# Kernel tuning notes

Hardware: AMD Instinct MI355X
Metric: run time of the kernel (lower is better)

The kernel has to match this reference:

```python
import jax, jax.numpy as jnp
import numpy as np

EPS = 1e-5


def setup_inputs() -> dict:
    key = jax.random.key(0)
    ks = jax.random.split(key, 8)
    B, C, D, H, O, E = 256, 64, 256, 4096, 256, 4
    x = jax.random.normal(ks[0], (B, C, D), dtype=jnp.float32)
    mask_ids = jax.random.randint(ks[1], (B, C), 0, 16)
    projection_idx = jax.random.randint(ks[2], (C,), 0, E)
    W1 = jax.random.normal(ks[3], (E, D, H), dtype=jnp.float32) * 0.02
    b1 = jnp.zeros((E, H), dtype=jnp.float32)
    gamma = jnp.ones((E, H), dtype=jnp.float32)
    beta = jnp.zeros((E, H), dtype=jnp.float32)
    W2 = jax.random.normal(ks[4], (E, H, O), dtype=jnp.float32) * 0.02
    b2 = jnp.zeros((E, O), dtype=jnp.float32)
    return {"x": x, "mask_ids": mask_ids, "projection_idx": projection_idx,
            "W1": W1, "b1": b1, "gamma": gamma, "beta": beta, "W2": W2, "b2": b2}


def reference(x, mask_ids, projection_idx, W1, b1, gamma, beta, W2, b2):
    # x: [B, C, D]; projection_idx: [C] routes each channel to one of E experts.
    # Disjoint masks => the original zeros + masked '+=' is a partition-assign.
    B, C, D = x.shape
    E, _, H = W1.shape
    # Per-channel expert params (gather once, shared over batch).
    h = jnp.einsum('bcd,cdh->bch', x, W1[projection_idx]) + b1[projection_idx]
    # BatchNorm1d in training mode: batch stats over the tokens of each expert
    # (the original flattens the selected [B, |mask|] tokens for BN).
    seg = jnp.broadcast_to(projection_idx[None, :], (B, C)).reshape(-1)  # [B*C]
    hf = h.reshape(B * C, H)
    cnt = jax.ops.segment_sum(jnp.ones((B * C,), h.dtype), seg, num_segments=E)
    cnt = jnp.maximum(cnt, 1.0)
    s1 = jax.ops.segment_sum(hf, seg, num_segments=E)            # [E, H]
    s2 = jax.ops.segment_sum(hf * hf, seg, num_segments=E)       # [E, H]
    mean = s1 / cnt[:, None]
    var = s2 / cnt[:, None] - mean * mean                        # biased var (train-mode BN)
    inv = jax.lax.rsqrt(var + EPS)
    hn = (h - mean[projection_idx]) * (inv[projection_idx] * gamma[projection_idx]) + beta[projection_idx]
    a = jax.nn.relu(hn)
    out = jnp.einsum('bch,cho->bco', a, W2[projection_idx]) + b2[projection_idx]
    return out, mask_ids
```

## Files before the change

kernel.cpp:

```cpp
#include <hip/hip_runtime.h>

typedef unsigned short u16;
typedef unsigned int   u32;
typedef __attribute__((ext_vector_type(8))) short s16x8;
typedef __attribute__((ext_vector_type(4))) float f32x4;
typedef __attribute__((ext_vector_type(4))) u32   u32x4;

#define DEV static __device__ __forceinline__

static constexpr int B_ = 256, C_ = 64, D_ = 256, H_ = 4096, O_ = 256, E_ = 4;

DEV u16 f2bf(float f) {
  u32 u = __builtin_bit_cast(u32, f);
  u += 0x7fffu + ((u >> 16) & 1u);
  return (u16)(u >> 16);
}
DEV float bf2f(u16 u) { return __builtin_bit_cast(float, (u32)u << 16); }

DEV void async16(const u16* g, u16* l) {
  __builtin_amdgcn_global_load_lds(
      (const __attribute__((address_space(1))) void*)g,
      (__attribute__((address_space(3))) void*)l, 16, 0, 0);
}

DEV int xcd_swz(int bid, int nwg) { return (bid & 7) * (nwg >> 3) + (bid >> 3); }

__global__ void k_prep(const float* __restrict__ x, u16* __restrict__ xb,
                       const float* __restrict__ W1, u16* __restrict__ w1t,
                       const float* __restrict__ W2, u16* __restrict__ w2t,
                       const int* __restrict__ mask, float* __restrict__ maskOut,
                       const int* __restrict__ proj, int* __restrict__ perm) {
  __shared__ float tile[64][65];
  const int bx = blockIdx.x, tid = threadIdx.x;
  if (bx < 2048) {
    const int i = bx * 256 + tid;
    const f32x4 a = ((const f32x4*)x)[2 * i];
    const f32x4 b = ((const f32x4*)x)[2 * i + 1];
    u32x4 o;
    o[0] = (u32)f2bf(a[0]) | ((u32)f2bf(a[1]) << 16);
    o[1] = (u32)f2bf(a[2]) | ((u32)f2bf(a[3]) << 16);
    o[2] = (u32)f2bf(b[0]) | ((u32)f2bf(b[1]) << 16);
    o[3] = (u32)f2bf(b[2]) | ((u32)f2bf(b[3]) << 16);
    ((u32x4*)xb)[i] = o;
    return;
  }
  if (bx < 4096) {
    const bool w1 = bx < 3072;
    const int R  = w1 ? D_ : H_;
    const int Cc = w1 ? H_ : O_;
    const float* s0 = w1 ? W1 : W2;
    u16* d0 = w1 ? w1t : w2t;
    int b = bx - (w1 ? 2048 : 3072);
    const int nct = Cc >> 6, nrt = R >> 6;
    const int ct = b % nct; b /= nct;
    const int rt = b % nrt; const int e = b / nrt;
    const float* s = s0 + (size_t)e * R * Cc;
    u16* d = d0 + (size_t)e * R * Cc;
    const int tx = tid & 63, ty = tid >> 6;
    #pragma unroll
    for (int i = 0; i < 64; i += 4)
      tile[i + ty][tx] = s[(size_t)(rt * 64 + i + ty) * Cc + ct * 64 + tx];
    __syncthreads();
    #pragma unroll
    for (int i = 0; i < 64; i += 4) {
      const int cc = i + ty;
      d[(size_t)(ct * 64 + cc) * R + rt * 64 + tx] = f2bf(tile[tx][cc]);
    }
    return;
  }
  if (bx < 4104) {
    const int i = (bx - 4096) * 256 + tid;
    #pragma unroll
    for (int j = 0; j < 8; ++j) maskOut[i * 8 + j] = (float)mask[i * 8 + j];
    return;
  }
  if (tid < C_) {
    const int e = proj[tid];
    int rank = 0;
    for (int c2 = 0; c2 < C_; ++c2) {
      const int e2 = proj[c2];
      rank += (e2 < e) || (e2 == e && c2 < tid);
    }
    perm[rank] = tid;
  }
}

__global__ __launch_bounds__(256, 3)
void k_gemm1(const u16* __restrict__ A, const u16* __restrict__ Bw,
             const int* __restrict__ proj, const int* __restrict__ perm,
             const float* __restrict__ bias,
             u16* __restrict__ outH, float* __restrict__ s1p, float* __restrict__ s2p) {
  constexpr int BM = 128, BN = 128, BK = 32, KT = D_ / BK;
  constexpr int SA = BM * BK / 8, SB = BN * BK / 8;
  constexpr int BUF = (SA + SB) * 8;
  __shared__ __align__(16) u16 lds[3 * BUF];
  __shared__ float stash[2][4][16][2];
  const int tid = threadIdx.x, l = tid & 63, w = tid >> 6, wm = w >> 1, wn = w & 1;

  int bid = xcd_swz(blockIdx.x, gridDim.x);
  constexpr int NT = H_ / BN, BT = B_ / BM;
  const int nt = bid % NT; bid /= NT;
  const int bt = bid % BT; const int ci = bid / BT;
  const int c = perm[ci];
  const int e = proj[c];

  const size_t rsA = (size_t)C_ * D_;
  const u16* Ab = A + (size_t)c * D_ + (size_t)bt * BM * rsA;
  const u16* Bb = Bw + ((size_t)e * H_ + (size_t)nt * BN) * D_;

  f32x4 acc[4][4] = {};

  auto stage = [&](int kt) {
    const int k0 = kt * BK;
    u16* dst = lds + (kt % 3) * BUF;
    #pragma unroll
    for (int i = 0; i < 2; ++i) {
      const int s = i * 256 + tid, row = s >> 2, j = (s & 3) ^ ((row >> 1) & 3);
      async16(Ab + (size_t)row * rsA + k0 + j * 8, dst + s * 8);
    }
    #pragma unroll
    for (int i = 0; i < 2; ++i) {
      const int s = i * 256 + tid, col = s >> 2, j = (s & 3) ^ ((col >> 1) & 3);
      async16(Bb + (size_t)col * D_ + k0 + j * 8, dst + SA * 8 + s * 8);
    }
  };

  stage(0);
  asm volatile("" ::: "memory");
  stage(1);
  asm volatile("s_waitcnt vmcnt(4)" ::: "memory");
  __builtin_amdgcn_s_barrier();

  #pragma unroll
  for (int kt = 0; kt < KT; ++kt) {
    if (kt + 2 < KT) stage(kt + 2);
    const u16* bufA = lds + (kt % 3) * BUF;
    const u16* bufB = bufA + SA * 8;
    s16x8 av[4], bv[4];
    #pragma unroll
    for (int m = 0; m < 4; ++m) {
      const int r = wm * 64 + m * 16 + (l & 15), p = (l >> 4) ^ ((r >> 1) & 3);
      av[m] = *(const s16x8*)(bufA + (r * 4 + p) * 8);
    }
    #pragma unroll
    for (int n = 0; n < 4; ++n) {
      const int cc = wn * 64 + n * 16 + (l & 15), p = (l >> 4) ^ ((cc >> 1) & 3);
      bv[n] = *(const s16x8*)(bufB + (cc * 4 + p) * 8);
    }
    #pragma unroll
    for (int m = 0; m < 4; ++m)
      #pragma unroll
      for (int n = 0; n < 4; ++n)
        acc[m][n] = __builtin_amdgcn_mfma_f32_16x16x32_bf16(av[m], bv[n], acc[m][n], 0, 0, 0);
    if (kt + 2 < KT)      asm volatile("s_waitcnt vmcnt(4) lgkmcnt(0)" ::: "memory");
    else if (kt + 1 < KT) asm volatile("s_waitcnt vmcnt(0) lgkmcnt(0)" ::: "memory");
    if (kt + 1 < KT) __builtin_amdgcn_s_barrier();
  }
  __syncthreads();

  u16* ldsOut = lds;
  float p1s[4], p2s[4];
  #pragma unroll
  for (int n = 0; n < 4; ++n) {
    const int colL = wn * 64 + n * 16 + (l & 15);
    const int colg = nt * BN + colL;
    const float bval = bias[e * H_ + colg];
    float p1 = 0.f, p2 = 0.f;
    #pragma unroll
    for (int m = 0; m < 4; ++m) {
      const int rbase = wm * 64 + m * 16 + (l >> 4) * 4;
      #pragma unroll
      for (int i = 0; i < 4; ++i) {
        const float v = acc[m][n][i] + bval;
        p1 += v; p2 += v * v;
        const int row = rbase + i;
        const int phys = (colL >> 3) ^ (row & 15);
        ldsOut[row * 128 + phys * 8 + (colL & 7)] = f2bf(v);
      }
    }
    p1 += __shfl_xor(p1, 16); p1 += __shfl_xor(p1, 32);
    p2 += __shfl_xor(p2, 16); p2 += __shfl_xor(p2, 32);
    if (wm == 1 && l < 16) { stash[wn][n][l & 15][0] = p1; stash[wn][n][l & 15][1] = p2; }
    p1s[n] = p1; p2s[n] = p2;
  }
  __syncthreads();
  if (wm == 0 && l < 16) {
    const int rowp = c * 2 + bt;
    #pragma unroll
    for (int n = 0; n < 4; ++n) {
      const int colg = nt * BN + wn * 64 + n * 16 + (l & 15);
      s1p[(size_t)rowp * H_ + colg] = p1s[n] + stash[wn][n][l & 15][0];
      s2p[(size_t)rowp * H_ + colg] = p2s[n] + stash[wn][n][l & 15][1];
    }
  }
  u16* outB = outH + (((size_t)c * NT + nt) * B_ + (size_t)bt * BM) * 128;
  #pragma unroll
  for (int pass = 0; pass < 8; ++pass) {
    const int row = pass * 16 + (tid >> 4), sl = tid & 15;
    const u32x4 v = *(const u32x4*)(ldsOut + row * 128 + ((sl ^ (row & 15)) * 8));
    *(u32x4*)(outB + (size_t)row * 128 + sl * 8) = v;
  }
}

__global__ void k_finalize(const float* __restrict__ s1p, const float* __restrict__ s2p,
                           const int* __restrict__ proj, const float* __restrict__ gamma,
                           const float* __restrict__ beta,
                           u16* __restrict__ sclB, u16* __restrict__ shfB) {
  const int i = blockIdx.x * 256 + threadIdx.x;
  const int e = i >> 12;
  const int hcol = i & 4095;
  int cn = 0;
  float q1 = 0.f, q2 = 0.f;
  for (int c = 0; c < C_; ++c) {
    if (proj[c] == e) {
      ++cn;
      q1 += s1p[(size_t)(c * 2) * H_ + hcol] + s1p[(size_t)(c * 2 + 1) * H_ + hcol];
      q2 += s2p[(size_t)(c * 2) * H_ + hcol] + s2p[(size_t)(c * 2 + 1) * H_ + hcol];
    }
  }
  const float cnt = fmaxf((float)cn * (float)B_, 1.f);
  const float mean = q1 / cnt;
  const float var = q2 / cnt - mean * mean;
  const float sc = rsqrtf(var + 1e-5f) * gamma[i];
  sclB[i] = f2bf(sc);
  shfB[i] = f2bf(beta[i] - mean * sc);
}

__global__ __launch_bounds__(256, 2)
void k_gemm2(const u16* __restrict__ A, const u16* __restrict__ Bw,
             const int* __restrict__ proj, const int* __restrict__ perm,
             const float* __restrict__ b2,
             const u16* __restrict__ scB, const u16* __restrict__ shB,
             float* __restrict__ outF, float* __restrict__ partial) {
  constexpr int KS = 2;
  constexpr int BM = 64, BN = 256, BK = 32, KH = H_ / KS, KT = KH / BK;
  constexpr int SA = BM * BK / 8, SB = BN * BK / 8;
  constexpr int BUF = (SA + SB) * 8;
  __shared__ __align__(16) u16 lds[2 * BUF + 2 * KH];
  u16* stS = lds + 2 * BUF;
  u16* stT = stS + KH;
  const int tid = threadIdx.x, l = tid & 63, w = tid >> 6;

  int bid = xcd_swz(blockIdx.x, gridDim.x);
  const int ks = bid & 1; bid >>= 1;
  const int bt = bid & 3; const int ci = bid >> 2;
  const int c = perm[ci];
  const int e = proj[c];

  const u16* Ab = A + ((size_t)c * 32 * B_ + (size_t)bt * BM) * 128;
  const u16* Bb = Bw + (size_t)e * O_ * H_ + (size_t)ks * KH;
  const u16* scE = scB + e * H_ + ks * KH;
  const u16* shE = shB + e * H_ + ks * KH;

  f32x4 acc[4][4] = {};
  s16x8 h0[1], h1[1], b0r[4], b1r[4];

  auto Aissue = [&](int kt, s16x8 (&hs)[1]) {
    const int row = tid >> 2, j = (tid & 3) ^ ((row >> 1) & 3);
    const int kg = ks * KH + kt * BK + j * 8;
    hs[0] = *(const s16x8*)(Ab + (size_t)(kg >> 7) * (B_ * 128) + row * 128 + (kg & 127));
  };
  auto Bissue = [&](int kt, s16x8 (&bs)[4]) {
    const int k0 = kt * BK;
    #pragma unroll
    for (int i = 0; i < 4; ++i) {
      const int s = i * 256 + tid, col = s >> 2, j = (s & 3) ^ ((col >> 1) & 3);
      bs[i] = *(const s16x8*)(Bb + (size_t)col * H_ + k0 + j * 8);
    }
  };
  auto Awrite = [&](int kt, s16x8 (&hs)[1]) {
    u16* dst = lds + (kt & 1) * BUF;
    const int k0 = kt * BK;
    const int row = tid >> 2, j = (tid & 3) ^ ((row >> 1) & 3);
    const s16x8 sv = *(const s16x8*)(stS + k0 + j * 8);
    const s16x8 tv = *(const s16x8*)(stT + k0 + j * 8);
    u32x4 o;
    #pragma unroll
    for (int jj = 0; jj < 4; ++jj) {
      const float v0 = fmaxf(bf2f((u16)hs[0][2 * jj]) * bf2f((u16)sv[2 * jj]) + bf2f((u16)tv[2 * jj]), 0.f);
      const float v1 = fmaxf(bf2f((u16)hs[0][2 * jj + 1]) * bf2f((u16)sv[2 * jj + 1]) + bf2f((u16)tv[2 * jj + 1]), 0.f);
      o[jj] = (u32)f2bf(v0) | ((u32)f2bf(v1) << 16);
    }
    *(u32x4*)(dst + tid * 8) = o;
  };
  auto Bwrite = [&](int kt, s16x8 (&bs)[4]) {
    u16* dst = lds + (kt & 1) * BUF + SA * 8;
    #pragma unroll
    for (int i = 0; i < 4; ++i) {
      const int s = i * 256 + tid;
      *(u32x4*)(dst + s * 8) = __builtin_bit_cast(u32x4, bs[i]);
    }
  };
  auto Compute = [&](int kt) {
    const u16* bufA = lds + (kt & 1) * BUF;
    const u16* bufB = bufA + SA * 8;
    s16x8 av[4], bv[4];
    #pragma unroll
    for (int m = 0; m < 4; ++m) {
      const int r = m * 16 + (l & 15), p = (l >> 4) ^ ((r >> 1) & 3);
      av[m] = *(const s16x8*)(bufA + (r * 4 + p) * 8);
    }
    #pragma unroll
    for (int n = 0; n < 4; ++n) {
      const int cc = w * 64 + n * 16 + (l & 15), p = (l >> 4) ^ ((cc >> 1) & 3);
      bv[n] = *(const s16x8*)(bufB + (cc * 4 + p) * 8);
    }
    #pragma unroll
    for (int m = 0; m < 4; ++m)
      #pragma unroll
      for (int n = 0; n < 4; ++n)
        acc[m][n] = __builtin_amdgcn_mfma_f32_16x16x32_bf16(av[m], bv[n], acc[m][n], 0, 0, 0);
  };

  for (int q = tid; q < KH / 4; q += 256) {
    if (q < KH / 8) async16(scE + q * 8, stS + q * 8);
    else            async16(shE + (q - KH / 8) * 8, stT + (q - KH / 8) * 8);
  }
  Aissue(0, h0); Bissue(0, b0r);
  Aissue(1, h1); Bissue(1, b1r);
  asm volatile("s_waitcnt vmcnt(0)" ::: "memory");
  __builtin_amdgcn_s_barrier();
  Awrite(0, h0); Bwrite(0, b0r);
  asm volatile("s_waitcnt lgkmcnt(0)" ::: "memory");
  __builtin_amdgcn_s_barrier();

  #pragma unroll 1
  for (int kt = 0; kt + 3 < KT; kt += 2) {
    Aissue(kt + 2, h0); Bissue(kt + 2, b0r);
    Compute(kt);
    Awrite(kt + 1, h1); Bwrite(kt + 1, b1r);
    asm volatile("s_waitcnt lgkmcnt(0)" ::: "memory");
    __builtin_amdgcn_s_barrier();
    Aissue(kt + 3, h1); Bissue(kt + 3, b1r);
    Compute(kt + 1);
    Awrite(kt + 2, h0); Bwrite(kt + 2, b0r);
    asm volatile("s_waitcnt lgkmcnt(0)" ::: "memory");
    __builtin_amdgcn_s_barrier();
  }

  Compute(KT - 2);
  Awrite(KT - 1, h1); Bwrite(KT - 1, b1r);
  asm volatile("s_waitcnt lgkmcnt(0)" ::: "memory");
  __builtin_amdgcn_s_barrier();
  Compute(KT - 1);

  float* dstF = ks ? partial : outF;
  #pragma unroll
  for (int n = 0; n < 4; ++n) {
    const int colg = w * 64 + n * 16 + (l & 15);
    const float bval = ks ? 0.f : b2[e * O_ + colg];
    #pragma unroll
    for (int m = 0; m < 4; ++m) {
      #pragma unroll
      for (int i = 0; i < 4; ++i) {
        const int rg = bt * BM + m * 16 + (l >> 4) * 4 + i;
        dstF[((size_t)rg * C_ + c) * O_ + colg] = acc[m][n][i] + bval;
      }
    }
  }
}

__global__ void k_combine(float* __restrict__ out, const float* __restrict__ partial) {
  const int gi = blockIdx.x * 256 + threadIdx.x;
  const size_t b = (size_t)gi * 2;
  f32x4 a0 = ((const f32x4*)out)[b], a1 = ((const f32x4*)out)[b + 1];
  const f32x4 p0 = ((const f32x4*)partial)[b], p1 = ((const f32x4*)partial)[b + 1];
  #pragma unroll
  for (int j = 0; j < 4; ++j) { a0[j] += p0[j]; a1[j] += p1[j]; }
  ((f32x4*)out)[b] = a0; ((f32x4*)out)[b + 1] = a1;
}

extern "C" void kernel_launch(void* const* d_in, const int* in_sizes, int n_in,
                              void* d_out, int out_size, void* d_ws, size_t ws_size,
                              hipStream_t stream) {
  const float* x     = (const float*)d_in[0];
  const int*   mask  = (const int*)d_in[1];
  const int*   proj  = (const int*)d_in[2];
  const float* W1    = (const float*)d_in[3];
  const float* b1    = (const float*)d_in[4];
  const float* gamma = (const float*)d_in[5];
  const float* beta  = (const float*)d_in[6];
  const float* W2    = (const float*)d_in[7];
  const float* b2    = (const float*)d_in[8];
  float* out = (float*)d_out;

  char* ws = (char*)d_ws;
  size_t off = 0;
  u16* hbuf = (u16*)(ws + off); off += (size_t)B_ * C_ * H_ * 2;
  u16* xb   = (u16*)(ws + off); off += (size_t)B_ * C_ * D_ * 2;
  u16* w1t  = (u16*)(ws + off); off += (size_t)E_ * D_ * H_ * 2;
  float* partial = (float*)xb;
  u16* w2t  = (u16*)(ws + off); off += (size_t)E_ * H_ * O_ * 2;
  float* s1p = (float*)(ws + off); off += (size_t)2 * C_ * H_ * 4;
  float* s2p = (float*)(ws + off); off += (size_t)2 * C_ * H_ * 4;
  u16* sclB = (u16*)(ws + off); off += (size_t)E_ * H_ * 2;
  u16* shfB = (u16*)(ws + off); off += (size_t)E_ * H_ * 2;
  int* perm = (int*)(ws + off); off += 256;

  k_prep<<<4105, 256, 0, stream>>>(x, xb, W1, w1t, W2, w2t, mask,
                                   out + (size_t)B_ * C_ * O_, proj, perm);

  k_gemm1<<<C_ * 2 * 32, 256, 0, stream>>>(xb, w1t, proj, perm, b1, hbuf, s1p, s2p);

  k_finalize<<<E_ * H_ / 256, 256, 0, stream>>>(s1p, s2p, proj, gamma, beta, sclB, shfB);

  k_gemm2<<<512, 256, 0, stream>>>(hbuf, w2t, proj, perm, b2, sclB, shfB, out, partial);

  k_combine<<<B_ * C_ * O_ / 8 / 256, 256, 0, stream>>>(out, partial);
}
```

Before: 151.9 us.

## Enlarge gemm1 M tile to full batch and drop per-half stat partials

Doubles the gemm1 block tile in M from 128 to 256 rows so each block covers the whole batch for its channel, which halves the grid and the re-loading of W1 tiles. Per-channel BN partial sums no longer need two batch-half rows, so finalize reads half as much. The output epilogue now stages the bf16 tile through LDS in two halves to fit the existing buffer. In exchange it raises accumulator registers (8x4 fragments), lowers the occupancy target from 3 to 2 blocks per CU, and leaves fewer blocks to fill the GPU.

```diff
diff --git a/kernel.cpp b/kernel.cpp
--- a/kernel.cpp
+++ b/kernel.cpp
@@ -85,12 +85,12 @@
   }
 }
 
-__global__ __launch_bounds__(256, 3)
+__global__ __launch_bounds__(256, 2)
 void k_gemm1(const u16* __restrict__ A, const u16* __restrict__ Bw,
              const int* __restrict__ proj, const int* __restrict__ perm,
              const float* __restrict__ bias,
              u16* __restrict__ outH, float* __restrict__ s1p, float* __restrict__ s2p) {
-  constexpr int BM = 128, BN = 128, BK = 32, KT = D_ / BK;
+  constexpr int BM = 256, BN = 128, BK = 32, KT = D_ / BK;
   constexpr int SA = BM * BK / 8, SB = BN * BK / 8;
   constexpr int BUF = (SA + SB) * 8;
   __shared__ __align__(16) u16 lds[3 * BUF];
@@ -98,23 +98,22 @@
   const int tid = threadIdx.x, l = tid & 63, w = tid >> 6, wm = w >> 1, wn = w & 1;
 
   int bid = xcd_swz(blockIdx.x, gridDim.x);
-  constexpr int NT = H_ / BN, BT = B_ / BM;
-  const int nt = bid % NT; bid /= NT;
-  const int bt = bid % BT; const int ci = bid / BT;
+  constexpr int NT = H_ / BN;
+  const int nt = bid % NT; const int ci = bid / NT;
   const int c = perm[ci];
   const int e = proj[c];
 
   const size_t rsA = (size_t)C_ * D_;
-  const u16* Ab = A + (size_t)c * D_ + (size_t)bt * BM * rsA;
+  const u16* Ab = A + (size_t)c * D_;
   const u16* Bb = Bw + ((size_t)e * H_ + (size_t)nt * BN) * D_;
 
-  f32x4 acc[4][4] = {};
+  f32x4 acc[8][4] = {};
 
   auto stage = [&](int kt) {
     const int k0 = kt * BK;
     u16* dst = lds + (kt % 3) * BUF;
     #pragma unroll
-    for (int i = 0; i < 2; ++i) {
+    for (int i = 0; i < 4; ++i) {
       const int s = i * 256 + tid, row = s >> 2, j = (s & 3) ^ ((row >> 1) & 3);
       async16(Ab + (size_t)row * rsA + k0 + j * 8, dst + s * 8);
     }
@@ -128,7 +127,7 @@
   stage(0);
   asm volatile("" ::: "memory");
   stage(1);
-  asm volatile("s_waitcnt vmcnt(4)" ::: "memory");
+  asm volatile("s_waitcnt vmcnt(6)" ::: "memory");
   __builtin_amdgcn_s_barrier();
 
   #pragma unroll
@@ -136,10 +135,10 @@
     if (kt + 2 < KT) stage(kt + 2);
     const u16* bufA = lds + (kt % 3) * BUF;
     const u16* bufB = bufA + SA * 8;
-    s16x8 av[4], bv[4];
-    #pragma unroll
-    for (int m = 0; m < 4; ++m) {
-      const int r = wm * 64 + m * 16 + (l & 15), p = (l >> 4) ^ ((r >> 1) & 3);
+    s16x8 av[8], bv[4];
+    #pragma unroll
+    for (int m = 0; m < 8; ++m) {
+      const int r = wm * 128 + m * 16 + (l & 15), p = (l >> 4) ^ ((r >> 1) & 3);
       av[m] = *(const s16x8*)(bufA + (r * 4 + p) * 8);
     }
     #pragma unroll
@@ -148,36 +147,28 @@
       bv[n] = *(const s16x8*)(bufB + (cc * 4 + p) * 8);
     }
     #pragma unroll
-    for (int m = 0; m < 4; ++m)
+    for (int m = 0; m < 8; ++m)
       #pragma unroll
       for (int n = 0; n < 4; ++n)
         acc[m][n] = __builtin_amdgcn_mfma_f32_16x16x32_bf16(av[m], bv[n], acc[m][n], 0, 0, 0);
-    if (kt + 2 < KT)      asm volatile("s_waitcnt vmcnt(4) lgkmcnt(0)" ::: "memory");
+    if (kt + 2 < KT)      asm volatile("s_waitcnt vmcnt(6) lgkmcnt(0)" ::: "memory");
     else if (kt + 1 < KT) asm volatile("s_waitcnt vmcnt(0) lgkmcnt(0)" ::: "memory");
     if (kt + 1 < KT) __builtin_amdgcn_s_barrier();
   }
-  __syncthreads();
-
-  u16* ldsOut = lds;
+
   float p1s[4], p2s[4];
   #pragma unroll
   for (int n = 0; n < 4; ++n) {
     const int colL = wn * 64 + n * 16 + (l & 15);
-    const int colg = nt * BN + colL;
-    const float bval = bias[e * H_ + colg];
+    const float bval = bias[e * H_ + nt * BN + colL];
     float p1 = 0.f, p2 = 0.f;
     #pragma unroll
-    for (int m = 0; m < 4; ++m) {
-      const int rbase = wm * 64 + m * 16 + (l >> 4) * 4;
+    for (int m = 0; m < 8; ++m)
       #pragma unroll
       for (int i = 0; i < 4; ++i) {
         const float v = acc[m][n][i] + bval;
         p1 += v; p2 += v * v;
-        const int row = rbase + i;
-        const int phys = (colL >> 3) ^ (row & 15);
-        ldsOut[row * 128 + phys * 8 + (colL & 7)] = f2bf(v);
       }
-    }
     p1 += __shfl_xor(p1, 16); p1 += __shfl_xor(p1, 32);
     p2 += __shfl_xor(p2, 16); p2 += __shfl_xor(p2, 32);
     if (wm == 1 && l < 16) { stash[wn][n][l & 15][0] = p1; stash[wn][n][l & 15][1] = p2; }
@@ -185,20 +176,41 @@
   }
   __syncthreads();
   if (wm == 0 && l < 16) {
-    const int rowp = c * 2 + bt;
     #pragma unroll
     for (int n = 0; n < 4; ++n) {
       const int colg = nt * BN + wn * 64 + n * 16 + (l & 15);
-      s1p[(size_t)rowp * H_ + colg] = p1s[n] + stash[wn][n][l & 15][0];
-      s2p[(size_t)rowp * H_ + colg] = p2s[n] + stash[wn][n][l & 15][1];
-    }
-  }
-  u16* outB = outH + (((size_t)c * NT + nt) * B_ + (size_t)bt * BM) * 128;
+      s1p[(size_t)c * H_ + colg] = p1s[n] + stash[wn][n][l & 15][0];
+      s2p[(size_t)c * H_ + colg] = p2s[n] + stash[wn][n][l & 15][1];
+    }
+  }
+
+  u16* ldsOut = lds;
   #pragma unroll
-  for (int pass = 0; pass < 8; ++pass) {
-    const int row = pass * 16 + (tid >> 4), sl = tid & 15;
-    const u32x4 v = *(const u32x4*)(ldsOut + row * 128 + ((sl ^ (row & 15)) * 8));
-    *(u32x4*)(outB + (size_t)row * 128 + sl * 8) = v;
+  for (int hh = 0; hh < 2; ++hh) {
+    __syncthreads();
+    if (wm == hh) {
+      #pragma unroll
+      for (int n = 0; n < 4; ++n) {
+        const int colL = wn * 64 + n * 16 + (l & 15);
+        const float bval = bias[e * H_ + nt * BN + colL];
+        #pragma unroll
+        for (int m = 0; m < 8; ++m)
+          #pragma unroll
+          for (int i = 0; i < 4; ++i) {
+            const int r2 = m * 16 + (l >> 4) * 4 + i;
+            const int phys = (colL >> 3) ^ (r2 & 15);
+            ldsOut[r2 * 128 + phys * 8 + (colL & 7)] = f2bf(acc[m][n][i] + bval);
+          }
+      }
+    }
+    __syncthreads();
+    u16* outB = outH + (((size_t)c * NT + nt) * B_ + hh * 128) * 128;
+    #pragma unroll
+    for (int pass = 0; pass < 8; ++pass) {
+      const int row = pass * 16 + (tid >> 4), sl = tid & 15;
+      const u32x4 v = *(const u32x4*)(ldsOut + row * 128 + ((sl ^ (row & 15)) * 8));
+      *(u32x4*)(outB + (size_t)row * 128 + sl * 8) = v;
+    }
   }
 }
 
@@ -214,8 +226,8 @@
   for (int c = 0; c < C_; ++c) {
     if (proj[c] == e) {
       ++cn;
-      q1 += s1p[(size_t)(c * 2) * H_ + hcol] + s1p[(size_t)(c * 2 + 1) * H_ + hcol];
-      q2 += s2p[(size_t)(c * 2) * H_ + hcol] + s2p[(size_t)(c * 2 + 1) * H_ + hcol];
+      q1 += s1p[(size_t)c * H_ + hcol];
+      q2 += s2p[(size_t)c * H_ + hcol];
     }
   }
   const float cnt = fmaxf((float)cn * (float)B_, 1.f);
@@ -391,8 +403,8 @@
   u16* w1t  = (u16*)(ws + off); off += (size_t)E_ * D_ * H_ * 2;
   float* partial = (float*)xb;
   u16* w2t  = (u16*)(ws + off); off += (size_t)E_ * H_ * O_ * 2;
-  float* s1p = (float*)(ws + off); off += (size_t)2 * C_ * H_ * 4;
-  float* s2p = (float*)(ws + off); off += (size_t)2 * C_ * H_ * 4;
+  float* s1p = (float*)(ws + off); off += (size_t)C_ * H_ * 4;
+  float* s2p = (float*)(ws + off); off += (size_t)C_ * H_ * 4;
   u16* sclB = (u16*)(ws + off); off += (size_t)E_ * H_ * 2;
   u16* shfB = (u16*)(ws + off); off += (size_t)E_ * H_ * 2;
   int* perm = (int*)(ws + off); off += 256;
@@ -400,7 +412,7 @@
   k_prep<<<4105, 256, 0, stream>>>(x, xb, W1, w1t, W2, w2t, mask,
                                    out + (size_t)B_ * C_ * O_, proj, perm);
 
-  k_gemm1<<<C_ * 2 * 32, 256, 0, stream>>>(xb, w1t, proj, perm, b1, hbuf, s1p, s2p);
+  k_gemm1<<<C_ * 32, 256, 0, stream>>>(xb, w1t, proj, perm, b1, hbuf, s1p, s2p);
 
   k_finalize<<<E_ * H_ / 256, 256, 0, stream>>>(s1p, s2p, proj, gamma, beta, sclB, shfB);
 
```

After: 162.8 us. +7.2%, slower.
